# Kernel tuning notes

Measured on AMD Instinct MI355X. Metric: run time of the kernel, lower is better.

Reference implementation:

```python
import jax, jax.numpy as jnp
import numpy as np

W_LOSS = 10.0
THRESHOLD = 1.0
ACOS_EPS = 1e-7


def _normalize(v, eps=1e-8):
    n = jnp.linalg.norm(v, axis=-1, keepdims=True)
    return v / jnp.maximum(n, eps)


def quat_to_rotmat(q):
    # q: (..., 4) in (w, x, y, z) order, as in Zhou et al. / EPN repo
    q = _normalize(q)
    w, x, y, z = q[..., 0], q[..., 1], q[..., 2], q[..., 3]
    R = jnp.stack([
        1 - 2 * (y * y + z * z), 2 * (x * y - z * w), 2 * (x * z + y * w),
        2 * (x * y + z * w), 1 - 2 * (x * x + z * z), 2 * (y * z - x * w),
        2 * (x * z - y * w), 2 * (y * z + x * w), 1 - 2 * (x * x + y * y),
    ], axis=-1)
    return R.reshape(q.shape[:-1] + (3, 3))


def acos_safe(x):
    return jnp.arccos(jnp.clip(x, -1.0 + ACOS_EPS, 1.0 - ACOS_EPS))


def angle_from_R(R):
    # R: (..., 3, 3) -> geodesic angle via trace
    tr = jnp.trace(R, axis1=-2, axis2=-1)
    return acos_safe(0.5 * (tr - 1.0))


def setup_inputs() -> dict:
    key = jax.random.key(0)
    k1, k2, k3, k4, k5 = jax.random.split(key, 5)
    B, NA, NR = 32768, 60, 4
    wts = jax.random.normal(k1, (B, NA), dtype=jnp.float32)
    label = jax.random.randint(k2, (B,), 0, NA, dtype=jnp.int64)
    y = jax.random.normal(k3, (B, NR, NA), dtype=jnp.float32)
    # gt_R and anchors are valid rotation matrices (via random quaternions)
    gt_R = quat_to_rotmat(jax.random.normal(k4, (B, NA, 4), dtype=jnp.float32))
    anchors = quat_to_rotmat(jax.random.normal(k5, (NA, 4), dtype=jnp.float32))
    return {"wts": wts, "label": label, "y": y, "gt_R": gt_R, "anchors": anchors}


def reference(wts, label, y, gt_R, anchors):
    b, na = wts.shape
    nr = y.shape[1]
    true_R = gt_R[:, 29]  # (b, 3, 3)

    # --- CrossEntropyLoss branch (classifier) ---
    logp = jax.nn.log_softmax(wts, axis=1)
    cls_loss = -jnp.mean(jnp.take_along_axis(logp, label[:, None], axis=1))
    preds = jnp.argmax(wts, axis=1)  # (b,)
    r_acc = jnp.mean((preds == label).astype(jnp.float32))

    # --- anchor-wise predicted rotations ---
    # y (b, nr, na) -> (b, na, nr) -> (b, na, 3, 3)
    pred_RAnchor = quat_to_rotmat(jnp.swapaxes(y, 1, 2))

    gt_bias = angle_from_R(gt_R)  # (b, na)
    mask = (gt_bias < THRESHOLD).astype(gt_R.dtype)[:, :, None, None]
    l2_loss = jnp.sum(jnp.square(gt_R * mask - pred_RAnchor * mask))
    loss = cls_loss + W_LOSS * l2_loss

    # --- final predicted rotation: gather best anchor, compose with anchor rot ---
    sel = jnp.take_along_axis(pred_RAnchor, preds[:, None, None, None], axis=1)[:, 0]  # (b,3,3)
    pred_R = jnp.einsum('bij,bjk->bik', anchors[preds], sel)

    # --- mean angular error ---
    ang_err = angle_from_R(jnp.einsum('bij,bkj->bik', pred_R, true_R))  # (b,)

    return (loss, cls_loss, W_LOSS * l2_loss, r_acc, ang_err)
```

## Files before the change

### kernel.cpp

```cpp
#include <hip/hip_runtime.h>
#include <math.h>

constexpr int Bc  = 32768;
constexpr int NAc = 60;
constexpr int NRc = 4;

constexpr int NP     = Bc * NAc;
constexpr int TILE   = 256;
constexpr int L2_BLOCKS  = NP / TILE;
constexpr int CLS_BLOCKS = Bc / 4;
constexpr int TOT_BLOCKS = L2_BLOCKS + CLS_BLOCKS;

#define COS_ONE 0.5403023058681398f

__global__ __launch_bounds__(256) void mtl_fused(
    const float* __restrict__ wts,
    const int*   __restrict__ label,
    const float* __restrict__ y,
    const float* __restrict__ gt_R,
    const float* __restrict__ anchors,
    float*       __restrict__ out,
    float*       __restrict__ l2p,
    float*       __restrict__ lpp,
    float*       __restrict__ crp)
{
    const int tid  = threadIdx.x;
    const int lane = tid & 63;
    const int wave = tid >> 6;

    if (blockIdx.x < L2_BLOCKS) {
        __shared__ float4 sg4[TILE * 9 / 4];
        float* sg = (float*)sg4;
        const int tile = blockIdx.x;

        const float4* gbase = (const float4*)(gt_R + (size_t)tile * (TILE * 9));
        sg4[tid] = gbase[tid];
        sg4[tid + 256] = gbase[tid + 256];
        if (tid < TILE * 9 / 4 - 512) sg4[tid + 512] = gbase[tid + 512];

        const int p = tile * TILE + tid;
        const int b = p / NAc;
        const int a = p - b * NAc;
        const float* yb = y + (size_t)b * (NRc * NAc) + a;
        float qw = yb[0 * NAc];
        float qx = yb[1 * NAc];
        float qy = yb[2 * NAc];
        float qz = yb[3 * NAc];
        __syncthreads();

        const float* g = sg + tid * 9;
        float g0 = g[0], g1 = g[1], g2 = g[2];
        float g3 = g[3], g4 = g[4], g5 = g[5];
        float g6 = g[6], g7 = g[7], g8 = g[8];

        float n   = sqrtf(qw * qw + qx * qx + qy * qy + qz * qz);
        float inv = 1.0f / fmaxf(n, 1e-8f);
        qw *= inv; qx *= inv; qy *= inv; qz *= inv;

        float R00 = 1.0f - 2.0f * (qy * qy + qz * qz);
        float R01 = 2.0f * (qx * qy - qz * qw);
        float R02 = 2.0f * (qx * qz + qy * qw);
        float R10 = 2.0f * (qx * qy + qz * qw);
        float R11 = 1.0f - 2.0f * (qx * qx + qz * qz);
        float R12 = 2.0f * (qy * qz - qx * qw);
        float R20 = 2.0f * (qx * qz - qy * qw);
        float R21 = 2.0f * (qy * qz + qx * qw);
        float R22 = 1.0f - 2.0f * (qx * qx + qy * qy);

        float acc = 0.0f;
        float xb = 0.5f * (g0 + g4 + g8 - 1.0f);
        if (xb > COS_ONE) {
            float d0 = g0 - R00, d1 = g1 - R01, d2 = g2 - R02;
            float d3 = g3 - R10, d4 = g4 - R11, d5 = g5 - R12;
            float d6 = g6 - R20, d7 = g7 - R21, d8 = g8 - R22;
            acc = d0 * d0 + d1 * d1 + d2 * d2
                + d3 * d3 + d4 * d4 + d5 * d5
                + d6 * d6 + d7 * d7 + d8 * d8;
        }

        for (int off = 32; off; off >>= 1) acc += __shfl_xor(acc, off, 64);
        __shared__ float sred[4];
        if (lane == 0) sred[wave] = acc;
        __syncthreads();
        if (tid == 0) l2p[tile] = sred[0] + sred[1] + sred[2] + sred[3];

    } else {
        const int cb = blockIdx.x - L2_BLOCKS;
        const int b  = cb * 4 + wave;

        float w = -INFINITY;
        if (lane < NAc) w = wts[(size_t)b * NAc + lane];
        float mv = w;
        int   mi = lane;
        for (int off = 32; off; off >>= 1) {
            float ov = __shfl_xor(mv, off, 64);
            int   oi = __shfl_xor(mi, off, 64);
            if (ov > mv || (ov == mv && oi < mi)) { mv = ov; mi = oi; }
        }
        float e  = (lane < NAc) ? expf(w - mv) : 0.0f;
        float se = e;
        for (int off = 32; off; off >>= 1) se += __shfl_xor(se, off, 64);
        float lse  = mv + logf(se);
        int   lab  = label[b];
        float wlab = __shfl(w, lab, 64);

        __shared__ float s_lp[4], s_cr[4];
        if (lane == 0) {
            s_lp[wave] = wlab - lse;
            s_cr[wave] = (mi == lab) ? 1.0f : 0.0f;
        }

        if (lane == mi) {
            const float* ybp = y + (size_t)b * (NRc * NAc) + mi;
            float qw = ybp[0 * NAc];
            float qx = ybp[1 * NAc];
            float qy = ybp[2 * NAc];
            float qz = ybp[3 * NAc];
            float n   = sqrtf(qw * qw + qx * qx + qy * qy + qz * qz);
            float inv = 1.0f / fmaxf(n, 1e-8f);
            qw *= inv; qx *= inv; qy *= inv; qz *= inv;
            float R00 = 1.0f - 2.0f * (qy * qy + qz * qz);
            float R01 = 2.0f * (qx * qy - qz * qw);
            float R02 = 2.0f * (qx * qz + qy * qw);
            float R10 = 2.0f * (qx * qy + qz * qw);
            float R11 = 1.0f - 2.0f * (qx * qx + qz * qz);
            float R12 = 2.0f * (qy * qz - qx * qw);
            float R20 = 2.0f * (qx * qz - qy * qw);
            float R21 = 2.0f * (qy * qz + qx * qw);
            float R22 = 1.0f - 2.0f * (qx * qx + qy * qy);

            const float* A = anchors + (size_t)mi * 9;
            float a0 = A[0], a1 = A[1], a2 = A[2];
            float a3 = A[3], a4 = A[4], a5 = A[5];
            float a6 = A[6], a7 = A[7], a8 = A[8];
            float P00 = a0 * R00 + a1 * R10 + a2 * R20;
            float P01 = a0 * R01 + a1 * R11 + a2 * R21;
            float P02 = a0 * R02 + a1 * R12 + a2 * R22;
            float P10 = a3 * R00 + a4 * R10 + a5 * R20;
            float P11 = a3 * R01 + a4 * R11 + a5 * R21;
            float P12 = a3 * R02 + a4 * R12 + a5 * R22;
            float P20 = a6 * R00 + a7 * R10 + a8 * R20;
            float P21 = a6 * R01 + a7 * R11 + a8 * R21;
            float P22 = a6 * R02 + a7 * R12 + a8 * R22;
            const float* tR = gt_R + ((size_t)b * NAc + 29) * 9;
            float tr = P00 * tR[0] + P01 * tR[1] + P02 * tR[2]
                     + P10 * tR[3] + P11 * tR[4] + P12 * tR[5]
                     + P20 * tR[6] + P21 * tR[7] + P22 * tR[8];
            float cx = 0.5f * (tr - 1.0f);
            cx = fminf(fmaxf(cx, -1.0f + 1e-7f), 1.0f - 1e-7f);
            out[4 + b] = acosf(cx);
        }

        __syncthreads();
        if (tid == 0) {
            lpp[cb] = s_lp[0] + s_lp[1] + s_lp[2] + s_lp[3];
            crp[cb] = s_cr[0] + s_cr[1] + s_cr[2] + s_cr[3];
        }
    }
}

__global__ __launch_bounds__(256) void mtl_final(
    const float* __restrict__ l2p,
    const float* __restrict__ lpp,
    const float* __restrict__ crp,
    float*       __restrict__ out)
{
    const int tid  = threadIdx.x;
    const int lane = tid & 63;
    const int wave = tid >> 6;

    double l2 = 0.0, lp = 0.0, cr = 0.0;

    const float4* l2p4 = (const float4*)l2p;
    const float4* lpp4 = (const float4*)lpp;
    const float4* crp4 = (const float4*)crp;
    for (int i = tid; i < L2_BLOCKS / 4; i += 256) {
        float4 v = l2p4[i];
        l2 += (double)v.x + (double)v.y + (double)v.z + (double)v.w;
    }
    for (int i = tid; i < CLS_BLOCKS / 4; i += 256) {
        float4 v = lpp4[i];
        lp += (double)v.x + (double)v.y + (double)v.z + (double)v.w;
        float4 u = crp4[i];
        cr += (double)u.x + (double)u.y + (double)u.z + (double)u.w;
    }

    for (int off = 32; off; off >>= 1) {
        l2 += __shfl_xor(l2, off, 64);
        lp += __shfl_xor(lp, off, 64);
        cr += __shfl_xor(cr, off, 64);
    }
    __shared__ double s_l2[4], s_lp[4], s_cr[4];
    if (lane == 0) { s_l2[wave] = l2; s_lp[wave] = lp; s_cr[wave] = cr; }
    __syncthreads();
    if (tid == 0) {
        double t2 = s_l2[0] + s_l2[1] + s_l2[2] + s_l2[3];
        double tp = s_lp[0] + s_lp[1] + s_lp[2] + s_lp[3];
        double tc = s_cr[0] + s_cr[1] + s_cr[2] + s_cr[3];
        float cls = (float)(-tp / (double)Bc);
        float l2s = (float)(10.0 * t2);
        out[0] = cls + l2s;
        out[1] = cls;
        out[2] = l2s;
        out[3] = (float)(tc / (double)Bc);
    }
}

extern "C" void kernel_launch(void* const* d_in, const int* in_sizes, int n_in,
                              void* d_out, int out_size, void* d_ws, size_t ws_size,
                              hipStream_t stream) {
    const float* wts     = (const float*)d_in[0];
    const int*   label   = (const int*)d_in[1];
    const float* y       = (const float*)d_in[2];
    const float* gt_R    = (const float*)d_in[3];
    const float* anchors = (const float*)d_in[4];
    float* out = (float*)d_out;

    float* l2p = (float*)d_ws;
    float* lpp = l2p + L2_BLOCKS;
    float* crp = lpp + CLS_BLOCKS;

    mtl_fused<<<TOT_BLOCKS, 256, 0, stream>>>(wts, label, y, gt_R, anchors,
                                              out, l2p, lpp, crp);
    mtl_final<<<1, 256, 0, stream>>>(l2p, lpp, crp, out);
}
```

Baseline: 151.6 us.

## Use async global-to-LDS loads, two pairs per thread, and hoist classifier loads

The L2 branch now has each thread process two (batch, anchor) pairs and stages gt_R tiles into LDS with global_load_lds, so the copy no longer passes through registers. The classifier branch issues the y, label and true-rotation loads before the argmax reductions, with every lane computing its own rotation, and stages the anchors in shared memory. The aim is more bytes in flight per block and less serialized load latency after the argmax. In exchange LDS use per block roughly doubles, which can lower occupancy, and the classifier wave now does redundant rotation math on every lane.

```diff
diff --git a/kernel.cpp b/kernel.cpp
--- a/kernel.cpp
+++ b/kernel.cpp
@@ -5,13 +5,21 @@
 constexpr int NAc = 60;
 constexpr int NRc = 4;
 
-constexpr int NP     = Bc * NAc;
-constexpr int TILE   = 256;
-constexpr int L2_BLOCKS  = NP / TILE;
-constexpr int CLS_BLOCKS = Bc / 4;
-constexpr int TOT_BLOCKS = L2_BLOCKS + CLS_BLOCKS;
+constexpr int NP        = Bc * NAc;
+constexpr int TILE      = 256;
+constexpr int TPA       = 2;
+constexpr int PAIRS_PB  = TILE * TPA;
+constexpr int A_BLOCKS  = NP / PAIRS_PB;
+constexpr int B_BLOCKS  = Bc / 4;
+constexpr int TOT_BLOCKS = A_BLOCKS + B_BLOCKS;
 
 #define COS_ONE 0.5403023058681398f
+
+__device__ __forceinline__ void async_ld16(const float* g, float* l) {
+    __builtin_amdgcn_global_load_lds(
+        (const __attribute__((address_space(1))) void*)g,
+        (__attribute__((address_space(3))) void*)l, 16, 0, 0);
+}
 
 __global__ __launch_bounds__(256) void mtl_fused(
     const float* __restrict__ wts,
@@ -24,72 +32,111 @@
     float*       __restrict__ lpp,
     float*       __restrict__ crp)
 {
+    __shared__ __align__(16) float smem[PAIRS_PB * 9 + 16];
     const int tid  = threadIdx.x;
     const int lane = tid & 63;
     const int wave = tid >> 6;
 
-    if (blockIdx.x < L2_BLOCKS) {
-        __shared__ float4 sg4[TILE * 9 / 4];
-        float* sg = (float*)sg4;
-        const int tile = blockIdx.x;
-
-        const float4* gbase = (const float4*)(gt_R + (size_t)tile * (TILE * 9));
-        sg4[tid] = gbase[tid];
-        sg4[tid + 256] = gbase[tid + 256];
-        if (tid < TILE * 9 / 4 - 512) sg4[tid + 512] = gbase[tid + 512];
-
-        const int p = tile * TILE + tid;
-        const int b = p / NAc;
-        const int a = p - b * NAc;
-        const float* yb = y + (size_t)b * (NRc * NAc) + a;
-        float qw = yb[0 * NAc];
-        float qx = yb[1 * NAc];
-        float qy = yb[2 * NAc];
-        float qz = yb[3 * NAc];
-        __syncthreads();
-
-        const float* g = sg + tid * 9;
-        float g0 = g[0], g1 = g[1], g2 = g[2];
-        float g3 = g[3], g4 = g[4], g5 = g[5];
-        float g6 = g[6], g7 = g[7], g8 = g[8];
-
-        float n   = sqrtf(qw * qw + qx * qx + qy * qy + qz * qz);
-        float inv = 1.0f / fmaxf(n, 1e-8f);
-        qw *= inv; qx *= inv; qy *= inv; qz *= inv;
-
-        float R00 = 1.0f - 2.0f * (qy * qy + qz * qz);
-        float R01 = 2.0f * (qx * qy - qz * qw);
-        float R02 = 2.0f * (qx * qz + qy * qw);
-        float R10 = 2.0f * (qx * qy + qz * qw);
-        float R11 = 1.0f - 2.0f * (qx * qx + qz * qz);
-        float R12 = 2.0f * (qy * qz - qx * qw);
-        float R20 = 2.0f * (qx * qz - qy * qw);
-        float R21 = 2.0f * (qy * qz + qx * qw);
-        float R22 = 1.0f - 2.0f * (qx * qx + qy * qy);
+    if (blockIdx.x < A_BLOCKS) {
+        float* sg = smem;
+        const float* gbase = gt_R + (size_t)blockIdx.x * (PAIRS_PB * 9);
+
+        for (int c = wave; c < 18; c += 4)
+            async_ld16(gbase + c * 256 + lane * 4, sg + c * 256 + lane * 4);
+
+        float qw[TPA], qx[TPA], qy[TPA], qz[TPA];
+        #pragma unroll
+        for (int t = 0; t < TPA; ++t) {
+            int p = blockIdx.x * PAIRS_PB + t * TILE + tid;
+            int b = p / NAc;
+            int a = p - b * NAc;
+            const float* yb = y + (size_t)b * (NRc * NAc) + a;
+            qw[t] = yb[0 * NAc];
+            qx[t] = yb[1 * NAc];
+            qy[t] = yb[2 * NAc];
+            qz[t] = yb[3 * NAc];
+        }
+        __syncthreads();
 
         float acc = 0.0f;
-        float xb = 0.5f * (g0 + g4 + g8 - 1.0f);
-        if (xb > COS_ONE) {
-            float d0 = g0 - R00, d1 = g1 - R01, d2 = g2 - R02;
-            float d3 = g3 - R10, d4 = g4 - R11, d5 = g5 - R12;
-            float d6 = g6 - R20, d7 = g7 - R21, d8 = g8 - R22;
-            acc = d0 * d0 + d1 * d1 + d2 * d2
-                + d3 * d3 + d4 * d4 + d5 * d5
-                + d6 * d6 + d7 * d7 + d8 * d8;
+        #pragma unroll
+        for (int t = 0; t < TPA; ++t) {
+            const float* g = sg + t * (TILE * 9) + tid * 9;
+            float g0 = g[0], g1 = g[1], g2 = g[2];
+            float g3 = g[3], g4 = g[4], g5 = g[5];
+            float g6 = g[6], g7 = g[7], g8 = g[8];
+
+            float n   = sqrtf(qw[t]*qw[t] + qx[t]*qx[t] + qy[t]*qy[t] + qz[t]*qz[t]);
+            float inv = 1.0f / fmaxf(n, 1e-8f);
+            float w = qw[t] * inv, x = qx[t] * inv, yq = qy[t] * inv, z = qz[t] * inv;
+
+            float R00 = 1.0f - 2.0f * (yq * yq + z * z);
+            float R01 = 2.0f * (x * yq - z * w);
+            float R02 = 2.0f * (x * z + yq * w);
+            float R10 = 2.0f * (x * yq + z * w);
+            float R11 = 1.0f - 2.0f * (x * x + z * z);
+            float R12 = 2.0f * (yq * z - x * w);
+            float R20 = 2.0f * (x * z - yq * w);
+            float R21 = 2.0f * (yq * z + x * w);
+            float R22 = 1.0f - 2.0f * (x * x + yq * yq);
+
+            float xb = 0.5f * (g0 + g4 + g8 - 1.0f);
+            if (xb > COS_ONE) {
+                float d0 = g0 - R00, d1 = g1 - R01, d2 = g2 - R02;
+                float d3 = g3 - R10, d4 = g4 - R11, d5 = g5 - R12;
+                float d6 = g6 - R20, d7 = g7 - R21, d8 = g8 - R22;
+                acc += d0*d0 + d1*d1 + d2*d2
+                     + d3*d3 + d4*d4 + d5*d5
+                     + d6*d6 + d7*d7 + d8*d8;
+            }
         }
 
         for (int off = 32; off; off >>= 1) acc += __shfl_xor(acc, off, 64);
-        __shared__ float sred[4];
+        float* sred = smem + PAIRS_PB * 9;
         if (lane == 0) sred[wave] = acc;
         __syncthreads();
-        if (tid == 0) l2p[tile] = sred[0] + sred[1] + sred[2] + sred[3];
+        if (tid == 0) l2p[blockIdx.x] = sred[0] + sred[1] + sred[2] + sred[3];
 
     } else {
-        const int cb = blockIdx.x - L2_BLOCKS;
+        const int cb = blockIdx.x - A_BLOCKS;
         const int b  = cb * 4 + wave;
+        float* sA   = smem;
+        float* s_lp = smem + 544;
+        float* s_cr = smem + 548;
 
         float w = -INFINITY;
         if (lane < NAc) w = wts[(size_t)b * NAc + lane];
+        int lab = label[b];
+
+        const float* tRp = gt_R + ((size_t)b * NAc + 29) * 9;
+        float t0 = tRp[0], t1 = tRp[1], t2 = tRp[2];
+        float t3 = tRp[3], t4 = tRp[4], t5 = tRp[5];
+        float t6 = tRp[6], t7 = tRp[7], t8 = tRp[8];
+
+        float R00=0,R01=0,R02=0,R10=0,R11=0,R12=0,R20=0,R21=0,R22=0;
+        if (lane < NAc) {
+            const float* yb = y + (size_t)b * (NRc * NAc) + lane;
+            float qw = yb[0 * NAc];
+            float qx = yb[1 * NAc];
+            float qy = yb[2 * NAc];
+            float qz = yb[3 * NAc];
+            float n   = sqrtf(qw*qw + qx*qx + qy*qy + qz*qz);
+            float inv = 1.0f / fmaxf(n, 1e-8f);
+            qw *= inv; qx *= inv; qy *= inv; qz *= inv;
+            R00 = 1.0f - 2.0f * (qy*qy + qz*qz);
+            R01 = 2.0f * (qx*qy - qz*qw);
+            R02 = 2.0f * (qx*qz + qy*qw);
+            R10 = 2.0f * (qx*qy + qz*qw);
+            R11 = 1.0f - 2.0f * (qx*qx + qz*qz);
+            R12 = 2.0f * (qy*qz - qx*qw);
+            R20 = 2.0f * (qx*qz - qy*qw);
+            R21 = 2.0f * (qy*qz + qx*qw);
+            R22 = 1.0f - 2.0f * (qx*qx + qy*qy);
+        }
+
+        for (int i = tid; i < NAc * 9; i += 256) sA[i] = anchors[i];
+        __syncthreads();
+
         float mv = w;
         int   mi = lane;
         for (int off = 32; off; off >>= 1) {
@@ -101,51 +148,30 @@
         float se = e;
         for (int off = 32; off; off >>= 1) se += __shfl_xor(se, off, 64);
         float lse  = mv + logf(se);
-        int   lab  = label[b];
         float wlab = __shfl(w, lab, 64);
 
-        __shared__ float s_lp[4], s_cr[4];
         if (lane == 0) {
             s_lp[wave] = wlab - lse;
             s_cr[wave] = (mi == lab) ? 1.0f : 0.0f;
         }
 
         if (lane == mi) {
-            const float* ybp = y + (size_t)b * (NRc * NAc) + mi;
-            float qw = ybp[0 * NAc];
-            float qx = ybp[1 * NAc];
-            float qy = ybp[2 * NAc];
-            float qz = ybp[3 * NAc];
-            float n   = sqrtf(qw * qw + qx * qx + qy * qy + qz * qz);
-            float inv = 1.0f / fmaxf(n, 1e-8f);
-            qw *= inv; qx *= inv; qy *= inv; qz *= inv;
-            float R00 = 1.0f - 2.0f * (qy * qy + qz * qz);
-            float R01 = 2.0f * (qx * qy - qz * qw);
-            float R02 = 2.0f * (qx * qz + qy * qw);
-            float R10 = 2.0f * (qx * qy + qz * qw);
-            float R11 = 1.0f - 2.0f * (qx * qx + qz * qz);
-            float R12 = 2.0f * (qy * qz - qx * qw);
-            float R20 = 2.0f * (qx * qz - qy * qw);
-            float R21 = 2.0f * (qy * qz + qx * qw);
-            float R22 = 1.0f - 2.0f * (qx * qx + qy * qy);
-
-            const float* A = anchors + (size_t)mi * 9;
+            const float* A = sA + mi * 9;
             float a0 = A[0], a1 = A[1], a2 = A[2];
             float a3 = A[3], a4 = A[4], a5 = A[5];
             float a6 = A[6], a7 = A[7], a8 = A[8];
-            float P00 = a0 * R00 + a1 * R10 + a2 * R20;
-            float P01 = a0 * R01 + a1 * R11 + a2 * R21;
-            float P02 = a0 * R02 + a1 * R12 + a2 * R22;
-            float P10 = a3 * R00 + a4 * R10 + a5 * R20;
-            float P11 = a3 * R01 + a4 * R11 + a5 * R21;
-            float P12 = a3 * R02 + a4 * R12 + a5 * R22;
-            float P20 = a6 * R00 + a7 * R10 + a8 * R20;
-            float P21 = a6 * R01 + a7 * R11 + a8 * R21;
-            float P22 = a6 * R02 + a7 * R12 + a8 * R22;
-            const float* tR = gt_R + ((size_t)b * NAc + 29) * 9;
-            float tr = P00 * tR[0] + P01 * tR[1] + P02 * tR[2]
-                     + P10 * tR[3] + P11 * tR[4] + P12 * tR[5]
-                     + P20 * tR[6] + P21 * tR[7] + P22 * tR[8];
+            float P00 = a0*R00 + a1*R10 + a2*R20;
+            float P01 = a0*R01 + a1*R11 + a2*R21;
+            float P02 = a0*R02 + a1*R12 + a2*R22;
+            float P10 = a3*R00 + a4*R10 + a5*R20;
+            float P11 = a3*R01 + a4*R11 + a5*R21;
+            float P12 = a3*R02 + a4*R12 + a5*R22;
+            float P20 = a6*R00 + a7*R10 + a8*R20;
+            float P21 = a6*R01 + a7*R11 + a8*R21;
+            float P22 = a6*R02 + a7*R12 + a8*R22;
+            float tr = P00*t0 + P01*t1 + P02*t2
+                     + P10*t3 + P11*t4 + P12*t5
+                     + P20*t6 + P21*t7 + P22*t8;
             float cx = 0.5f * (tr - 1.0f);
             cx = fminf(fmaxf(cx, -1.0f + 1e-7f), 1.0f - 1e-7f);
             out[4 + b] = acosf(cx);
@@ -174,11 +200,11 @@
     const float4* l2p4 = (const float4*)l2p;
     const float4* lpp4 = (const float4*)lpp;
     const float4* crp4 = (const float4*)crp;
-    for (int i = tid; i < L2_BLOCKS / 4; i += 256) {
+    for (int i = tid; i < A_BLOCKS / 4; i += 256) {
         float4 v = l2p4[i];
         l2 += (double)v.x + (double)v.y + (double)v.z + (double)v.w;
     }
-    for (int i = tid; i < CLS_BLOCKS / 4; i += 256) {
+    for (int i = tid; i < B_BLOCKS / 4; i += 256) {
         float4 v = lpp4[i];
         lp += (double)v.x + (double)v.y + (double)v.z + (double)v.w;
         float4 u = crp4[i];
@@ -217,8 +243,8 @@
     float* out = (float*)d_out;
 
     float* l2p = (float*)d_ws;
-    float* lpp = l2p + L2_BLOCKS;
-    float* crp = lpp + CLS_BLOCKS;
+    float* lpp = l2p + A_BLOCKS;
+    float* crp = lpp + B_BLOCKS;
 
     mtl_fused<<<TOT_BLOCKS, 256, 0, stream>>>(wts, label, y, gt_R, anchors,
                                               out, l2p, lpp, crp);
```

Result: no change. 153.2 us (+1.0%).

## Merge L2 and classifier branches into one per-batch-row block kernel

Applied to the files above, without the earlier changes.

Restructures the fused kernel so each block handles 4 batch rows (one wavefront per row, one lane per anchor). Every block now computes the masked L2 term, the softmax/argmax, and the final rotation error together. The selected anchor's quaternion, anchor matrix and the true_R row are reused from registers and shared memory, so they are no longer re-read from global memory. This cuts the block count and removes the duplicate loads of y and gt_R[29]. In exchange, 4 of every 64 lanes sit idle and the block does more serial work.

```diff
diff --git a/kernel.cpp b/kernel.cpp
--- a/kernel.cpp
+++ b/kernel.cpp
@@ -3,17 +3,15 @@
 
 constexpr int Bc  = 32768;
 constexpr int NAc = 60;
-constexpr int NRc = 4;
 
-constexpr int NP     = Bc * NAc;
-constexpr int TILE   = 256;
-constexpr int L2_BLOCKS  = NP / TILE;
-constexpr int CLS_BLOCKS = Bc / 4;
-constexpr int TOT_BLOCKS = L2_BLOCKS + CLS_BLOCKS;
+constexpr int BPB  = 4;
+constexpr int NBLK = Bc / BPB;
+constexpr int ROWF = NAc * 9;
+constexpr int STG4 = BPB * ROWF / 4;
 
 #define COS_ONE 0.5403023058681398f
 
-__global__ __launch_bounds__(256) void mtl_fused(
+__global__ __launch_bounds__(256) void mtl_all(
     const float* __restrict__ wts,
     const int*   __restrict__ label,
     const float* __restrict__ y,
@@ -24,138 +22,116 @@
     float*       __restrict__ lpp,
     float*       __restrict__ crp)
 {
+    __shared__ __align__(16) float sg[BPB * ROWF + 16];
     const int tid  = threadIdx.x;
     const int lane = tid & 63;
     const int wave = tid >> 6;
+    const int b0   = blockIdx.x * BPB;
+    const int b    = b0 + wave;
 
-    if (blockIdx.x < L2_BLOCKS) {
-        __shared__ float4 sg4[TILE * 9 / 4];
-        float* sg = (float*)sg4;
-        const int tile = blockIdx.x;
+    const float4* gb4 = (const float4*)(gt_R + (size_t)b0 * ROWF);
+    float4* sg4 = (float4*)sg;
+    sg4[tid]       = gb4[tid];
+    sg4[tid + 256] = gb4[tid + 256];
+    if (tid < STG4 - 512) sg4[tid + 512] = gb4[tid + 512];
 
-        const float4* gbase = (const float4*)(gt_R + (size_t)tile * (TILE * 9));
-        sg4[tid] = gbase[tid];
-        sg4[tid + 256] = gbase[tid + 256];
-        if (tid < TILE * 9 / 4 - 512) sg4[tid + 512] = gbase[tid + 512];
+    const int a = lane;
+    int lab = label[b];
+    float w = -INFINITY;
+    float qw = 0, qx = 0, qy = 0, qz = 0;
+    float A0=0,A1=0,A2=0,A3=0,A4=0,A5=0,A6=0,A7=0,A8=0;
+    if (a < NAc) {
+        w = wts[(size_t)b * NAc + a];
+        const float* yb = y + (size_t)b * (4 * NAc) + a;
+        qw = yb[0 * NAc];
+        qx = yb[1 * NAc];
+        qy = yb[2 * NAc];
+        qz = yb[3 * NAc];
+        const float* Ar = anchors + a * 9;
+        A0 = Ar[0]; A1 = Ar[1]; A2 = Ar[2];
+        A3 = Ar[3]; A4 = Ar[4]; A5 = Ar[5];
+        A6 = Ar[6]; A7 = Ar[7]; A8 = Ar[8];
+    }
 
-        const int p = tile * TILE + tid;
-        const int b = p / NAc;
-        const int a = p - b * NAc;
-        const float* yb = y + (size_t)b * (NRc * NAc) + a;
-        float qw = yb[0 * NAc];
-        float qx = yb[1 * NAc];
-        float qy = yb[2 * NAc];
-        float qz = yb[3 * NAc];
-        __syncthreads();
+    float n   = sqrtf(qw*qw + qx*qx + qy*qy + qz*qz);
+    float inv = 1.0f / fmaxf(n, 1e-8f);
+    float pw = qw*inv, px = qx*inv, py = qy*inv, pz = qz*inv;
+    float R00 = 1.0f - 2.0f*(py*py + pz*pz);
+    float R01 = 2.0f*(px*py - pz*pw);
+    float R02 = 2.0f*(px*pz + py*pw);
+    float R10 = 2.0f*(px*py + pz*pw);
+    float R11 = 1.0f - 2.0f*(px*px + pz*pz);
+    float R12 = 2.0f*(py*pz - px*pw);
+    float R20 = 2.0f*(px*pz - py*pw);
+    float R21 = 2.0f*(py*pz + px*pw);
+    float R22 = 1.0f - 2.0f*(px*px + py*py);
 
-        const float* g = sg + tid * 9;
+    __syncthreads();
+
+    float acc = 0.0f;
+    if (a < NAc) {
+        const float* g = sg + wave * ROWF + a * 9;
         float g0 = g[0], g1 = g[1], g2 = g[2];
         float g3 = g[3], g4 = g[4], g5 = g[5];
         float g6 = g[6], g7 = g[7], g8 = g[8];
-
-        float n   = sqrtf(qw * qw + qx * qx + qy * qy + qz * qz);
-        float inv = 1.0f / fmaxf(n, 1e-8f);
-        qw *= inv; qx *= inv; qy *= inv; qz *= inv;
-
-        float R00 = 1.0f - 2.0f * (qy * qy + qz * qz);
-        float R01 = 2.0f * (qx * qy - qz * qw);
-        float R02 = 2.0f * (qx * qz + qy * qw);
-        float R10 = 2.0f * (qx * qy + qz * qw);
-        float R11 = 1.0f - 2.0f * (qx * qx + qz * qz);
-        float R12 = 2.0f * (qy * qz - qx * qw);
-        float R20 = 2.0f * (qx * qz - qy * qw);
-        float R21 = 2.0f * (qy * qz + qx * qw);
-        float R22 = 1.0f - 2.0f * (qx * qx + qy * qy);
-
-        float acc = 0.0f;
         float xb = 0.5f * (g0 + g4 + g8 - 1.0f);
         if (xb > COS_ONE) {
-            float d0 = g0 - R00, d1 = g1 - R01, d2 = g2 - R02;
-            float d3 = g3 - R10, d4 = g4 - R11, d5 = g5 - R12;
-            float d6 = g6 - R20, d7 = g7 - R21, d8 = g8 - R22;
-            acc = d0 * d0 + d1 * d1 + d2 * d2
-                + d3 * d3 + d4 * d4 + d5 * d5
-                + d6 * d6 + d7 * d7 + d8 * d8;
+            float d0 = g0-R00, d1 = g1-R01, d2 = g2-R02;
+            float d3 = g3-R10, d4 = g4-R11, d5 = g5-R12;
+            float d6 = g6-R20, d7 = g7-R21, d8 = g8-R22;
+            acc = d0*d0 + d1*d1 + d2*d2
+                + d3*d3 + d4*d4 + d5*d5
+                + d6*d6 + d7*d7 + d8*d8;
         }
+    }
 
-        for (int off = 32; off; off >>= 1) acc += __shfl_xor(acc, off, 64);
-        __shared__ float sred[4];
-        if (lane == 0) sred[wave] = acc;
-        __syncthreads();
-        if (tid == 0) l2p[tile] = sred[0] + sred[1] + sred[2] + sred[3];
+    float mv = w;
+    int   mi = lane;
+    for (int off = 32; off; off >>= 1) {
+        float ov = __shfl_xor(mv, off, 64);
+        int   oi = __shfl_xor(mi, off, 64);
+        if (ov > mv || (ov == mv && oi < mi)) { mv = ov; mi = oi; }
+    }
+    float e  = (a < NAc) ? expf(w - mv) : 0.0f;
+    float se = e;
+    for (int off = 32; off; off >>= 1) se += __shfl_xor(se, off, 64);
+    float lse  = mv + logf(se);
+    float wlab = __shfl(w, lab, 64);
 
-    } else {
-        const int cb = blockIdx.x - L2_BLOCKS;
-        const int b  = cb * 4 + wave;
+    if (lane == mi) {
+        float P00 = A0*R00 + A1*R10 + A2*R20;
+        float P01 = A0*R01 + A1*R11 + A2*R21;
+        float P02 = A0*R02 + A1*R12 + A2*R22;
+        float P10 = A3*R00 + A4*R10 + A5*R20;
+        float P11 = A3*R01 + A4*R11 + A5*R21;
+        float P12 = A3*R02 + A4*R12 + A5*R22;
+        float P20 = A6*R00 + A7*R10 + A8*R20;
+        float P21 = A6*R01 + A7*R11 + A8*R21;
+        float P22 = A6*R02 + A7*R12 + A8*R22;
+        const float* tR = sg + wave * ROWF + 29 * 9;
+        float tr = P00*tR[0] + P01*tR[1] + P02*tR[2]
+                 + P10*tR[3] + P11*tR[4] + P12*tR[5]
+                 + P20*tR[6] + P21*tR[7] + P22*tR[8];
+        float cx = 0.5f * (tr - 1.0f);
+        cx = fminf(fmaxf(cx, -1.0f + 1e-7f), 1.0f - 1e-7f);
+        out[4 + b] = acosf(cx);
+    }
 
-        float w = -INFINITY;
-        if (lane < NAc) w = wts[(size_t)b * NAc + lane];
-        float mv = w;
-        int   mi = lane;
-        for (int off = 32; off; off >>= 1) {
-            float ov = __shfl_xor(mv, off, 64);
-            int   oi = __shfl_xor(mi, off, 64);
-            if (ov > mv || (ov == mv && oi < mi)) { mv = ov; mi = oi; }
-        }
-        float e  = (lane < NAc) ? expf(w - mv) : 0.0f;
-        float se = e;
-        for (int off = 32; off; off >>= 1) se += __shfl_xor(se, off, 64);
-        float lse  = mv + logf(se);
-        int   lab  = label[b];
-        float wlab = __shfl(w, lab, 64);
+    for (int off = 32; off; off >>= 1) acc += __shfl_xor(acc, off, 64);
 
-        __shared__ float s_lp[4], s_cr[4];
-        if (lane == 0) {
-            s_lp[wave] = wlab - lse;
-            s_cr[wave] = (mi == lab) ? 1.0f : 0.0f;
-        }
-
-        if (lane == mi) {
-            const float* ybp = y + (size_t)b * (NRc * NAc) + mi;
-            float qw = ybp[0 * NAc];
-            float qx = ybp[1 * NAc];
-            float qy = ybp[2 * NAc];
-            float qz = ybp[3 * NAc];
-            float n   = sqrtf(qw * qw + qx * qx + qy * qy + qz * qz);
-            float inv = 1.0f / fmaxf(n, 1e-8f);
-            qw *= inv; qx *= inv; qy *= inv; qz *= inv;
-            float R00 = 1.0f - 2.0f * (qy * qy + qz * qz);
-            float R01 = 2.0f * (qx * qy - qz * qw);
-            float R02 = 2.0f * (qx * qz + qy * qw);
-            float R10 = 2.0f * (qx * qy + qz * qw);
-            float R11 = 1.0f - 2.0f * (qx * qx + qz * qz);
-            float R12 = 2.0f * (qy * qz - qx * qw);
-            float R20 = 2.0f * (qx * qz - qy * qw);
-            float R21 = 2.0f * (qy * qz + qx * qw);
-            float R22 = 1.0f - 2.0f * (qx * qx + qy * qy);
-
-            const float* A = anchors + (size_t)mi * 9;
-            float a0 = A[0], a1 = A[1], a2 = A[2];
-            float a3 = A[3], a4 = A[4], a5 = A[5];
-            float a6 = A[6], a7 = A[7], a8 = A[8];
-            float P00 = a0 * R00 + a1 * R10 + a2 * R20;
-            float P01 = a0 * R01 + a1 * R11 + a2 * R21;
-            float P02 = a0 * R02 + a1 * R12 + a2 * R22;
-            float P10 = a3 * R00 + a4 * R10 + a5 * R20;
-            float P11 = a3 * R01 + a4 * R11 + a5 * R21;
-            float P12 = a3 * R02 + a4 * R12 + a5 * R22;
-            float P20 = a6 * R00 + a7 * R10 + a8 * R20;
-            float P21 = a6 * R01 + a7 * R11 + a8 * R21;
-            float P22 = a6 * R02 + a7 * R12 + a8 * R22;
-            const float* tR = gt_R + ((size_t)b * NAc + 29) * 9;
-            float tr = P00 * tR[0] + P01 * tR[1] + P02 * tR[2]
-                     + P10 * tR[3] + P11 * tR[4] + P12 * tR[5]
-                     + P20 * tR[6] + P21 * tR[7] + P22 * tR[8];
-            float cx = 0.5f * (tr - 1.0f);
-            cx = fminf(fmaxf(cx, -1.0f + 1e-7f), 1.0f - 1e-7f);
-            out[4 + b] = acosf(cx);
-        }
-
-        __syncthreads();
-        if (tid == 0) {
-            lpp[cb] = s_lp[0] + s_lp[1] + s_lp[2] + s_lp[3];
-            crp[cb] = s_cr[0] + s_cr[1] + s_cr[2] + s_cr[3];
-        }
+    float* s_l2 = sg + BPB * ROWF;
+    float* s_lp = s_l2 + 4;
+    float* s_cr = s_lp + 4;
+    if (lane == 0) {
+        s_l2[wave] = acc;
+        s_lp[wave] = wlab - lse;
+        s_cr[wave] = (mi == lab) ? 1.0f : 0.0f;
+    }
+    __syncthreads();
+    if (tid == 0) {
+        l2p[blockIdx.x] = s_l2[0] + s_l2[1] + s_l2[2] + s_l2[3];
+        lpp[blockIdx.x] = s_lp[0] + s_lp[1] + s_lp[2] + s_lp[3];
+        crp[blockIdx.x] = s_cr[0] + s_cr[1] + s_cr[2] + s_cr[3];
     }
 }
 
@@ -170,19 +146,16 @@
     const int wave = tid >> 6;
 
     double l2 = 0.0, lp = 0.0, cr = 0.0;
-
     const float4* l2p4 = (const float4*)l2p;
     const float4* lpp4 = (const float4*)lpp;
     const float4* crp4 = (const float4*)crp;
-    for (int i = tid; i < L2_BLOCKS / 4; i += 256) {
+    for (int i = tid; i < NBLK / 4; i += 256) {
         float4 v = l2p4[i];
         l2 += (double)v.x + (double)v.y + (double)v.z + (double)v.w;
-    }
-    for (int i = tid; i < CLS_BLOCKS / 4; i += 256) {
-        float4 v = lpp4[i];
-        lp += (double)v.x + (double)v.y + (double)v.z + (double)v.w;
-        float4 u = crp4[i];
-        cr += (double)u.x + (double)u.y + (double)u.z + (double)u.w;
+        float4 u = lpp4[i];
+        lp += (double)u.x + (double)u.y + (double)u.z + (double)u.w;
+        float4 c = crp4[i];
+        cr += (double)c.x + (double)c.y + (double)c.z + (double)c.w;
     }
 
     for (int off = 32; off; off >>= 1) {
@@ -217,10 +190,10 @@
     float* out = (float*)d_out;
 
     float* l2p = (float*)d_ws;
-    float* lpp = l2p + L2_BLOCKS;
-    float* crp = lpp + CLS_BLOCKS;
+    float* lpp = l2p + NBLK;
+    float* crp = lpp + NBLK;
 
-    mtl_fused<<<TOT_BLOCKS, 256, 0, stream>>>(wts, label, y, gt_R, anchors,
-                                              out, l2p, lpp, crp);
+    mtl_all  <<<NBLK, 256, 0, stream>>>(wts, label, y, gt_R, anchors,
+                                        out, l2p, lpp, crp);
     mtl_final<<<1, 256, 0, stream>>>(l2p, lpp, crp, out);
 }
```

Result: faster. 140.0 us (-7.7%).
